# Kernel tuning notes

Hardware: AMD Instinct MI355X
Metric: run time of the kernel (lower is better)

## Reference

```python
import jax, jax.numpy as jnp
import numpy as np
from jax import lax

B, N, C, T = 8, 2000, 32, 12
K, F_CHEV, F_TIME = 3, 64, 64
LN_EPS = 1e-5


def setup_inputs() -> dict:
    key = jax.random.key(0)
    ks = jax.random.split(key, 20)
    s = 0.1
    return {
        "x": jax.random.normal(ks[0], (B, N, C, T), jnp.float32),
        "cheb_polys": jax.random.normal(ks[1], (K, N, N), jnp.float32) * 0.02,
        # temporal attention params
        "U1": jax.random.normal(ks[2], (N,), jnp.float32) * s,
        "U2": jax.random.normal(ks[3], (C, N), jnp.float32) * s,
        "U3": jax.random.normal(ks[4], (C,), jnp.float32) * s,
        "be": jax.random.normal(ks[5], (1, T, T), jnp.float32) * s,
        "Ve": jax.random.normal(ks[6], (T, T), jnp.float32) * s,
        # spatial attention params
        "W1": jax.random.normal(ks[7], (T,), jnp.float32) * s,
        "W2": jax.random.normal(ks[8], (C, T), jnp.float32) * s,
        "W3": jax.random.normal(ks[9], (C,), jnp.float32) * s,
        "bs": jax.random.normal(ks[10], (1, N, N), jnp.float32) * s,
        "Vs": jax.random.normal(ks[11], (N, N), jnp.float32) * (s / np.sqrt(N)),
        # Chebyshev conv params, stacked (K, C, F_chev)
        "Theta": jax.random.normal(ks[12], (K, C, F_CHEV), jnp.float32) * (1.0 / np.sqrt(C)),
        # time conv (1x3) and residual conv (1x1), NCHW/OIHW layout
        "tc_w": jax.random.normal(ks[13], (F_TIME, F_CHEV, 1, 3), jnp.float32) * (1.0 / np.sqrt(3 * F_CHEV)),
        "tc_b": jnp.zeros((F_TIME,), jnp.float32),
        "rc_w": jax.random.normal(ks[14], (F_TIME, C, 1, 1), jnp.float32) * (1.0 / np.sqrt(C)),
        "rc_b": jnp.zeros((F_TIME,), jnp.float32),
        # LayerNorm over nb_time_filter
        "ln_g": jnp.ones((F_TIME,), jnp.float32),
        "ln_b": jnp.zeros((F_TIME,), jnp.float32),
    }


def _conv2d(x, w, b, stride_t):
    # x: (B, Cin, N, T), w: (Cout, Cin, kh, kw)
    pad_w = (w.shape[3] - 1) // 2
    y = lax.conv_general_dilated(
        x, w, window_strides=(1, stride_t),
        padding=[(0, 0), (pad_w, pad_w)],
        dimension_numbers=("NCHW", "OIHW", "NCHW"))
    return y + b[None, :, None, None]


def reference(x, cheb_polys, U1, U2, U3, be, Ve, W1, W2, W3, bs, Vs,
              Theta, tc_w, tc_b, rc_w, rc_b, ln_g, ln_b):
    b, n, c, t = x.shape

    # ---- temporal attention: (B, T, T) ----
    lhs = jnp.einsum("bnct,n->btc", x, U1)              # x.permute(0,3,2,1) @ U1
    lhs = jnp.einsum("btc,cn->btn", lhs, U2)
    rhs = jnp.einsum("c,bnct->bnt", U3, x)
    E = jnp.einsum("ij,bjk->bik", Ve,
                   jax.nn.sigmoid(jnp.einsum("btn,bnu->btu", lhs, rhs) + be))
    temporal_At = jax.nn.softmax(E, axis=1)             # (B, T, T)

    # apply temporal attention
    x_TAt = jnp.matmul(x.reshape(b, n * c, t), temporal_At).reshape(b, n, c, t)

    # ---- spatial attention on x_TAt: (B, N, N) ----
    lhs_s = jnp.einsum("bnct,t->bnc", x_TAt, W1)
    lhs_s = jnp.einsum("bnc,ct->bnt", lhs_s, W2)
    rhs_s = jnp.einsum("c,bnct->btn", W3, x_TAt)        # (W3 @ x).transpose(-1,-2)
    S = jnp.einsum("ij,bjk->bik", Vs,
                   jax.nn.sigmoid(jnp.einsum("bnt,btm->bnm", lhs_s, rhs_s) + bs))
    spatial_At = jax.nn.softmax(S, axis=1)              # (B, N, N)

    # ---- Chebyshev graph conv with spatial attention ----
    # A[b,k,j,i] = cheb[k,j,i] * SAt[b,j,i]; out = relu(sum_k A^T x Theta_k)
    A = cheb_polys[None, :, :, :] * spatial_At[:, None, :, :]   # (B, K, N, N)
    h = jnp.einsum("bkji,bjct->bkitc", A, x)                    # (B, K, N, T, C)
    spatial_gcn = jax.nn.relu(jnp.einsum("bkitc,kcf->bift", h, Theta))  # (B, N, F, T)

    # ---- temporal conv + residual + LayerNorm ----
    time_out = _conv2d(spatial_gcn.transpose(0, 2, 1, 3), tc_w, tc_b, 1)  # (B, F_time, N, T')
    x_res = _conv2d(x.transpose(0, 2, 1, 3), rc_w, rc_b, 1)               # (B, F_time, N, T')
    z = jax.nn.relu(x_res + time_out).transpose(0, 3, 2, 1)               # (B, T', N, F_time)

    mu = jnp.mean(z, axis=-1, keepdims=True)
    var = jnp.mean((z - mu) ** 2, axis=-1, keepdims=True)
    zn = (z - mu) * lax.rsqrt(var + LN_EPS) * ln_g + ln_b

    return zn.transpose(0, 2, 3, 1)                                       # (B, N, F_time, T')
```

## Files before the change

kernel.cpp:

```cpp
#include <hip/hip_runtime.h>
#include <hip/hip_bf16.h>
#include <math.h>

#define B_ 8
#define N_ 2000
#define C_ 32
#define T_ 12
#define K_ 3
#define FC_ 64
#define FT_ 64
#define PW 2048

typedef short bf16x8 __attribute__((ext_vector_type(8)));
typedef float f32x4 __attribute__((ext_vector_type(4)));

__device__ __forceinline__ float sigmoidf(float v) { return 1.0f / (1.0f + __expf(-v)); }
__device__ __forceinline__ float bf2f(unsigned short u) {
    union { unsigned int i; float f; } v; v.i = ((unsigned int)u) << 16; return v.f;
}
__device__ __forceinline__ unsigned short f2bf(float f) {
    union { __hip_bfloat16 h; unsigned short u; } v; v.h = __float2bfloat16(f); return v.u;
}
typedef const __attribute__((address_space(1))) void* gas_t;
typedef __attribute__((address_space(3))) void* las_t;
__device__ __forceinline__ void gload16(const unsigned short* g, unsigned short* l) {
    __builtin_amdgcn_global_load_lds((gas_t)g, (las_t)l, 16, 0, 0);
}

__global__ __launch_bounds__(256) void k_tprep(const float* __restrict__ x, const float* __restrict__ U1,
                                               const float* __restrict__ U3,
                                               float* __restrict__ rhsT, float* __restrict__ plh) {
    int b = blockIdx.y, chunk = blockIdx.x;
    int tid = threadIdx.x;
    int nl = tid >> 5, c = tid & 31;
    int w = tid >> 6;
    float u3 = U3[c];
    float plA[12];
#pragma unroll
    for (int t = 0; t < 12; ++t) plA[t] = 0.f;
    for (int it = 0; it < 5; ++it) {
        int n = chunk * 40 + it * 8 + nl;
        const float* xp = x + ((size_t)(b * 2000 + n) * 32 + c) * 12;
        float4 v0 = *(const float4*)xp, v1 = *(const float4*)(xp + 4), v2 = *(const float4*)(xp + 8);
        float xv[12] = {v0.x, v0.y, v0.z, v0.w, v1.x, v1.y, v1.z, v1.w, v2.x, v2.y, v2.z, v2.w};
        float rv[12];
#pragma unroll
        for (int t = 0; t < 12; ++t) rv[t] = u3 * xv[t];
#pragma unroll
        for (int off = 16; off >= 1; off >>= 1)
#pragma unroll
            for (int t = 0; t < 12; ++t) rv[t] += __shfl_xor(rv[t], off);
        if (c == 0) {
#pragma unroll
            for (int t = 0; t < 12; ++t) rhsT[(size_t)(b * 2000 + n) * 12 + t] = rv[t];
        }
        float u1 = U1[n];
#pragma unroll
        for (int t = 0; t < 12; ++t) plA[t] += u1 * xv[t];
    }
#pragma unroll
    for (int t = 0; t < 12; ++t) plA[t] += __shfl_xor(plA[t], 32);
    __shared__ float accs[4][32][12];
    if ((tid & 63) < 32) {
#pragma unroll
        for (int t = 0; t < 12; ++t) accs[w][c][t] = plA[t];
    }
    __syncthreads();
    if (tid < 384) {
        int c2 = tid / 12, t2 = tid % 12;
        float s = accs[0][c2][t2] + accs[1][c2][t2] + accs[2][c2][t2] + accs[3][c2][t2];
        plh[((size_t)(b * 50 + chunk)) * 384 + tid] = s;
    }
}

__global__ __launch_bounds__(256) void k_tred(const float* __restrict__ plh, float* __restrict__ lhs1) {
    int b = blockIdx.x;
    for (int q = threadIdx.x; q < 384; q += 256) {
        const float* p = plh + (size_t)b * 50 * 384 + q;
        float s = 0.f;
        for (int ch = 0; ch < 50; ++ch) s += p[(size_t)ch * 384];
        int c = q / 12, t = q % 12;
        lhs1[(b * 12 + t) * 32 + c] = s;
    }
}

__global__ __launch_bounds__(256) void k_lhsT(const float* __restrict__ lhs1, const float* __restrict__ U2,
                                              float* __restrict__ lhsT) {
    int gid = blockIdx.x * 256 + threadIdx.x;
    if (gid >= B_ * T_ * N_) return;
    int n = gid % N_;
    int bt = gid / N_;
    const float* l1 = lhs1 + bt * C_;
    float a = 0.f;
#pragma unroll
    for (int c = 0; c < C_; ++c) a += l1[c] * U2[c * N_ + n];
    lhsT[gid] = a;
}

__global__ __launch_bounds__(256) void k_tatt1(const float* __restrict__ lhsT, const float* __restrict__ rhsT,
                                               float* __restrict__ pP) {
    int b = blockIdx.y, ch = blockIdx.x;
    int tid = threadIdx.x;
    int n0 = ch * 125;
    __shared__ float sL[12][128];
    __shared__ float sR[128][12];
    for (int q = tid; q < 12 * 125; q += 256) {
        int t = q / 125, nn = q % 125;
        sL[t][nn] = lhsT[(size_t)(b * 12 + t) * 2000 + n0 + nn];
    }
    for (int q = tid; q < 125 * 12; q += 256) {
        int nn = q / 12, t = q % 12;
        sR[nn][t] = rhsT[(size_t)(b * 2000 + n0 + nn) * 12 + t];
    }
    __syncthreads();
    if (tid < 144) {
        int tP = tid / 12, uP = tid % 12;
        float a = 0.f;
#pragma unroll 5
        for (int nn = 0; nn < 125; ++nn) a += sL[tP][nn] * sR[nn][uP];
        pP[(size_t)(b * 16 + ch) * 144 + tid] = a;
    }
}

__global__ __launch_bounds__(256) void k_tatt2(const float* __restrict__ pP, const float* __restrict__ be,
                                               const float* __restrict__ Ve, float* __restrict__ At) {
    int b = blockIdx.x, tid = threadIdx.x;
    __shared__ float sp[144], sE[144], mk[12], sk[12];
    int tP = tid / 12, uP = tid % 12;
    if (tid < 144) {
        float a = 0.f;
#pragma unroll
        for (int ch = 0; ch < 16; ++ch) a += pP[(size_t)(b * 16 + ch) * 144 + tid];
        sp[tid] = sigmoidf(a + be[tid]);
    }
    __syncthreads();
    if (tid < 144) {
        float e = 0.f;
#pragma unroll
        for (int j = 0; j < 12; ++j) e += Ve[tP * 12 + j] * sp[j * 12 + uP];
        sE[tid] = e;
    }
    __syncthreads();
    if (tid < 12) {
        float m = -1e30f;
#pragma unroll
        for (int i = 0; i < 12; ++i) m = fmaxf(m, sE[i * 12 + tid]);
        float s = 0.f;
#pragma unroll
        for (int i = 0; i < 12; ++i) s += __expf(sE[i * 12 + tid] - m);
        mk[tid] = m; sk[tid] = 1.0f / s;
    }
    __syncthreads();
    if (tid < 144) At[b * 144 + tid] = __expf(sE[tid] - mk[uP]) * sk[uP];
}

__global__ __launch_bounds__(256) void k_xsp(const float* __restrict__ x, const float* __restrict__ At,
                                             const float* __restrict__ W1, const float* __restrict__ W2,
                                             const float* __restrict__ W3,
                                             float* __restrict__ lhs_s, float* __restrict__ rhs_s) {
    int b = blockIdx.y, chunk = blockIdx.x;
    int tid = threadIdx.x, nl = tid >> 5, c = tid & 31;
    int n = chunk * 8 + nl;
    __shared__ float atl[144];
    __shared__ float w2l[384];
    __shared__ float w1l[12];
    if (tid < 144) atl[tid] = At[b * 144 + tid];
    if (tid >= 144 && tid < 156) w1l[tid - 144] = W1[tid - 144];
    for (int q = tid; q < 384; q += 256) w2l[q] = W2[q];
    __syncthreads();
    const float* xp = x + ((size_t)(b * 2000 + n) * 32 + c) * 12;
    float4 v0 = *(const float4*)xp, v1 = *(const float4*)(xp + 4), v2 = *(const float4*)(xp + 8);
    float xv[12] = {v0.x, v0.y, v0.z, v0.w, v1.x, v1.y, v1.z, v1.w, v2.x, v2.y, v2.z, v2.w};
    float xa[12];
#pragma unroll
    for (int t = 0; t < 12; ++t) {
        float s = 0.f;
#pragma unroll
        for (int u = 0; u < 12; ++u) s += xv[u] * atl[u * 12 + t];
        xa[t] = s;
    }
    float w3 = W3[c];
    float rv[12], lv[12];
    float l1 = 0.f;
#pragma unroll
    for (int t = 0; t < 12; ++t) l1 += xa[t] * w1l[t];
#pragma unroll
    for (int t = 0; t < 12; ++t) { rv[t] = w3 * xa[t]; lv[t] = l1 * w2l[c * 12 + t]; }
#pragma unroll
    for (int off = 16; off >= 1; off >>= 1)
#pragma unroll
        for (int t = 0; t < 12; ++t) { rv[t] += __shfl_xor(rv[t], off); lv[t] += __shfl_xor(lv[t], off); }
    if (c == 0) {
#pragma unroll
        for (int t = 0; t < 12; ++t) rhs_s[(size_t)(b * 12 + t) * 2000 + n] = rv[t];
#pragma unroll
        for (int t = 0; t < 12; ++t) lhs_s[(size_t)(b * 2000 + n) * 12 + t] = lv[t];
    }
}

__global__ __launch_bounds__(256) void k_wprep(const float* __restrict__ tc_w, const float* __restrict__ rc_w,
                                               float* __restrict__ tcwT, float* __restrict__ rcwT) {
    int gid = blockIdx.x * 256 + threadIdx.x;
    if (gid < 12288) {
        int fi = gid / 192, rem = gid % 192, f = rem / 3, d = rem % 3;
        tcwT[gid] = tc_w[(f * 64 + fi) * 3 + d];
    } else if (gid < 14336) {
        int q = gid - 12288;
        int c = q >> 6, f = q & 63;
        rcwT[q] = rc_w[f * 32 + c];
    }
}

__global__ __launch_bounds__(256) void k_vsb(const float* __restrict__ Vs, unsigned short* __restrict__ Vsb) {
    int gid = blockIdx.x * 256 + threadIdx.x;
    int row = gid >> 8, chunk = gid & 255;
    int p0 = chunk * 8;
    unsigned short o[8];
#pragma unroll
    for (int e = 0; e < 8; ++e) {
        int p = p0 + e;
        o[e] = (row < N_ && p < N_) ? f2bf(Vs[row * N_ + p]) : (unsigned short)0;
    }
    *(int4*)(Vsb + (size_t)row * PW + p0) = *(int4*)o;
}

__global__ __launch_bounds__(256) void k_chebT(const float* __restrict__ cheb, unsigned short* __restrict__ chebT) {
    int j0 = blockIdx.x * 64, i0 = blockIdx.y * 64, kk = blockIdx.z;
    __shared__ float Tl[64][65];
    int t = threadIdx.x;
    int rr = t >> 2, c0 = (t & 3) * 16;
    int j = j0 + rr;
#pragma unroll
    for (int e = 0; e < 16; ++e) {
        int i = i0 + c0 + e;
        Tl[rr][c0 + e] = (j < N_ && i < N_) ? cheb[(size_t)kk * 4000000 + (size_t)j * N_ + i] : 0.f;
    }
    __syncthreads();
    int l = t & 63, w = t >> 6;
    unsigned short o[16];
#pragma unroll
    for (int e = 0; e < 16; ++e) o[e] = f2bf(Tl[w * 16 + e][l]);
    unsigned short* dst = chebT + (size_t)kk * PW * PW + (size_t)(i0 + l) * PW + j0 + w * 16;
    *(int4*)dst = *(int4*)o;
    *(int4*)(dst + 8) = *(int4*)(o + 8);
}

__global__ __launch_bounds__(256) void k_xT(const float* __restrict__ x, unsigned short* __restrict__ xT) {
    int j0 = blockIdx.x * 64, r0 = blockIdx.y * 64, b = blockIdx.z;
    __shared__ float Tl[64][65];
    int t = threadIdx.x;
    int rr = t >> 2, c0 = (t & 3) * 16;
    int j = j0 + rr;
#pragma unroll
    for (int e = 0; e < 16; ++e) {
        int r = r0 + c0 + e;
        Tl[rr][c0 + e] = (j < N_) ? x[(size_t)(b * N_ + j) * 384 + r] : 0.f;
    }
    __syncthreads();
    int l = t & 63, w = t >> 6;
    unsigned short o[16];
#pragma unroll
    for (int e = 0; e < 16; ++e) o[e] = f2bf(Tl[w * 16 + e][l]);
    unsigned short* dst = xT + (size_t)b * 384 * PW + (size_t)(r0 + l) * PW + j0 + w * 16;
    *(int4*)dst = *(int4*)o;
    *(int4*)(dst + 8) = *(int4*)(o + 8);
}

__global__ __launch_bounds__(256) void k_sig(const float* __restrict__ lhs_s, const float* __restrict__ rhs_s,
                                             const float* __restrict__ bs, unsigned short* __restrict__ sigT) {
    int p0 = blockIdx.x * 64, i0 = blockIdx.y * 64, b = blockIdx.z;
    __shared__ float sL[64][12];
    __shared__ float sR[12][64];
    __shared__ float bsl[64][65];
    int t = threadIdx.x;
    for (int q = t; q < 768; q += 256) {
        int pp = q / 12, tt = q % 12;
        int p = p0 + pp;
        sL[pp][tt] = (p < N_) ? lhs_s[(b * N_ + p) * 12 + tt] : 0.f;
    }
    for (int q = t; q < 768; q += 256) {
        int tt = q >> 6, ii = q & 63;
        int i = i0 + ii;
        sR[tt][ii] = (i < N_) ? rhs_s[b * (T_ * N_) + tt * N_ + i] : 0.f;
    }
    {
        int pp = t >> 2, c0 = (t & 3) * 16;
        int p = p0 + pp;
        if (p < N_ && i0 + c0 + 15 < N_) {
            const float* src = bs + (size_t)p * N_ + i0 + c0;
#pragma unroll
            for (int e = 0; e < 16; e += 4) *(float4*)&bsl[pp][c0 + e] = *(const float4*)(src + e);
        } else {
#pragma unroll
            for (int e = 0; e < 16; ++e) {
                int i = i0 + c0 + e;
                bsl[pp][c0 + e] = (p < N_ && i < N_) ? bs[(size_t)p * N_ + i] : 0.f;
            }
        }
    }
    __syncthreads();
    int ii = t & 63, w = t >> 6;
    int i = i0 + ii;
    unsigned short o[16];
#pragma unroll
    for (int e = 0; e < 16; ++e) {
        int pl = w * 16 + e;
        int p = p0 + pl;
        float v = 0.f;
        if (p < N_ && i < N_) {
            float d = bsl[pl][ii];
#pragma unroll
            for (int tt = 0; tt < 12; ++tt) d += sL[pl][tt] * sR[tt][ii];
            v = sigmoidf(d);
        }
        o[e] = f2bf(v);
    }
    unsigned short* dst = sigT + (size_t)b * PW * PW + (size_t)i * PW + p0 + w * 16;
    *(int4*)dst = *(int4*)o;
    *(int4*)(dst + 8) = *(int4*)(o + 8);
}

__global__ __launch_bounds__(512) void k_gemm_S_mfma(const unsigned short* __restrict__ Vsb,
                                                     const unsigned short* __restrict__ sigT,
                                                     unsigned short* __restrict__ ST) {
    int lid = blockIdx.x + (blockIdx.y << 3) + (blockIdx.z << 6);
    int swz = (lid & 7) * 64 + (lid >> 3);
    int j0 = (swz & 7) * 256;
    int i0 = ((swz >> 3) & 7) * 256;
    int b = swz >> 6;
    const unsigned short* Ap = sigT + (size_t)b * PW * PW;
    __shared__ unsigned short As[2][16384];
    __shared__ unsigned short Bs[2][16384];
    int t = threadIdx.x, lane = t & 63, w = t >> 6;
    int wr = w >> 2, wc = w & 3;
    int l15 = lane & 15, kseg = lane >> 4;
    f32x4 acc[8][4];
#pragma unroll
    for (int m = 0; m < 8; ++m)
#pragma unroll
        for (int n = 0; n < 4; ++n)
#pragma unroll
            for (int q = 0; q < 4; ++q) acc[m][n][q] = 0.f;
    int srow = t >> 3;
    int schunk = ((t & 7) ^ (srow & 7)) * 8;
    const unsigned short* gA = Ap + (size_t)(i0 + srow) * PW + schunk;
    const unsigned short* gB = Vsb + (size_t)(j0 + srow) * PW + schunk;
    int ldw = w * 512;
#define SA_(buf_, kt_, h_) do { \
    gload16(gA + (size_t)((h_) * 128) * PW + (kt_) * 64, &As[buf_][(h_) * 8192 + ldw]); \
    gload16(gA + (size_t)((h_) * 128 + 64) * PW + (kt_) * 64, &As[buf_][(h_) * 8192 + 4096 + ldw]); \
} while (0)
#define SB_(buf_, kt_, h_) do { \
    gload16(gB + (size_t)((h_) * 128) * PW + (kt_) * 64, &Bs[buf_][(h_) * 8192 + ldw]); \
    gload16(gB + (size_t)((h_) * 128 + 64) * PW + (kt_) * 64, &Bs[buf_][(h_) * 8192 + 4096 + ldw]); \
} while (0)
#define RDA(dst, mh_, buf_) do { \
    _Pragma("unroll") for (int m = 0; m < 4; ++m) { \
        int R = wr * 128 + (mh_) * 64 + m * 16 + l15; \
        _Pragma("unroll") for (int kh = 0; kh < 2; ++kh) \
            dst[m][kh] = *(const bf16x8*)&As[buf_][R * 64 + (((kh * 4 + kseg) ^ (R & 7)) << 3)]; \
    } } while (0)
#define RDB(dst, nh_, buf_) do { \
    _Pragma("unroll") for (int n = 0; n < 2; ++n) { \
        int R = wc * 64 + (nh_) * 32 + n * 16 + l15; \
        _Pragma("unroll") for (int kh = 0; kh < 2; ++kh) \
            dst[n][kh] = *(const bf16x8*)&Bs[buf_][R * 64 + (((kh * 4 + kseg) ^ (R & 7)) << 3)]; \
    } } while (0)
#define LGKM0 do { asm volatile("s_waitcnt lgkmcnt(0)" ::: "memory"); __builtin_amdgcn_sched_barrier(0); } while (0)
#define MMA(av, bv, mh_, nh_) do { \
    __builtin_amdgcn_s_setprio(1); \
    _Pragma("unroll") for (int m = 0; m < 4; ++m) \
    _Pragma("unroll") for (int n = 0; n < 2; ++n) \
    _Pragma("unroll") for (int kh = 0; kh < 2; ++kh) \
        acc[m + (mh_) * 4][n + (nh_) * 2] = __builtin_amdgcn_mfma_f32_16x16x32_bf16( \
            av[m][kh], bv[n][kh], acc[m + (mh_) * 4][n + (nh_) * 2], 0, 0, 0); \
    __builtin_amdgcn_s_setprio(0); } while (0)
    SA_(0, 0, 0); SA_(0, 0, 1); SB_(0, 0, 0); SB_(0, 0, 1);
    for (int kt = 0; kt < 32; ++kt) {
        int buf = kt & 1, nbuf = buf ^ 1;
        bf16x8 aR[4][2], bR[2][2];
        asm volatile("s_waitcnt vmcnt(0)" ::: "memory");
        __builtin_amdgcn_s_barrier();
        __builtin_amdgcn_sched_barrier(0);
        if (kt + 1 < 32) { SA_(nbuf, kt + 1, 0); SA_(nbuf, kt + 1, 1); }
        RDA(aR, 0, buf); RDB(bR, 0, buf);
        LGKM0;
        MMA(aR, bR, 0, 0);
        __builtin_amdgcn_s_barrier();
        if (kt + 1 < 32) { SB_(nbuf, kt + 1, 0); SB_(nbuf, kt + 1, 1); }
        RDB(bR, 1, buf);
        LGKM0;
        MMA(aR, bR, 0, 1);
        __builtin_amdgcn_s_barrier();
        RDA(aR, 1, buf); RDB(bR, 0, buf);
        LGKM0;
        MMA(aR, bR, 1, 0);
        __builtin_amdgcn_s_barrier();
        RDB(bR, 1, buf);
        LGKM0;
        MMA(aR, bR, 1, 1);
    }
#undef SA_
#undef SB_
#undef RDA
#undef RDB
#undef LGKM0
#undef MMA
    unsigned short* Sp = ST + (size_t)b * PW * PW;
#pragma unroll
    for (int mi = 0; mi < 8; ++mi) {
        int row0 = i0 + wr * 128 + (mi >> 2) * 64 + (mi & 3) * 16 + (kseg << 2);
#pragma unroll
        for (int ni = 0; ni < 4; ++ni) {
            int col = j0 + wc * 64 + (ni >> 1) * 32 + (ni & 1) * 16 + l15;
#pragma unroll
            for (int q = 0; q < 4; ++q)
                Sp[(size_t)(row0 + q) * PW + col] = f2bf(acc[mi][ni][q]);
        }
    }
}

__global__ __launch_bounds__(256) void k_smrow(const unsigned short* __restrict__ ST,
                                               float* __restrict__ gm, float* __restrict__ gs) {
    int wid = threadIdx.x >> 6, lane = threadIdx.x & 63;
    int b = blockIdx.y;
    int i = blockIdx.x * 4 + wid;
    const unsigned short* rp = ST + (size_t)b * PW * PW + (size_t)i * PW;
    float vals[32];
    float m = -1e30f;
#pragma unroll
    for (int k = 0; k < 4; ++k) {
        int j0 = lane * 8 + k * 512;
        if (j0 < N_) {
            union { int4 v; unsigned short s[8]; } u;
            u.v = *(const int4*)(rp + j0);
#pragma unroll
            for (int e = 0; e < 8; ++e) {
                vals[k * 8 + e] = bf2f(u.s[e]);
                m = fmaxf(m, vals[k * 8 + e]);
            }
        } else {
#pragma unroll
            for (int e = 0; e < 8; ++e) vals[k * 8 + e] = -1e30f;
        }
    }
#pragma unroll
    for (int off = 32; off >= 1; off >>= 1) m = fmaxf(m, __shfl_xor(m, off));
    float s = 0.f;
#pragma unroll
    for (int k = 0; k < 32; ++k) s += __expf(vals[k] - m);
#pragma unroll
    for (int off = 32; off >= 1; off >>= 1) s += __shfl_xor(s, off);
    if (lane == 0) {
        gm[b * 2048 + i] = m;
        gs[b * 2048 + i] = 1.0f / s;
    }
}

__global__ __launch_bounds__(512) void k_gemm_cheb_mfma(const unsigned short* __restrict__ chebT,
                                                        const unsigned short* __restrict__ ST,
                                                        const float* __restrict__ gm, const float* __restrict__ gs,
                                                        const unsigned short* __restrict__ xT,
                                                        unsigned short* __restrict__ h2) {
    int bk = blockIdx.y;
    int b = bk / 3, kk = bk % 3;
    int i0 = blockIdx.x * 128;
    const unsigned short* Ac = chebT + (size_t)kk * PW * PW;
    const unsigned short* Sa = ST + (size_t)b * PW * PW;
    const unsigned short* Bx = xT + (size_t)b * 384 * PW;
    __shared__ unsigned short As[2][4096];
    __shared__ unsigned short Bs[2][12288];
    int t = threadIdx.x, lane = t & 63, w = t >> 6;
    int wr = w >> 2, wc = w & 3;
    f32x4 acc[4][6];
#pragma unroll
    for (int a = 0; a < 4; ++a)
#pragma unroll
        for (int c = 0; c < 6; ++c)
#pragma unroll
            for (int q = 0; q < 4; ++q) acc[a][c][q] = 0.f;
    int arow = t >> 2, aq = t & 3;
    const unsigned short* gc = Ac + (size_t)(i0 + arow) * PW + aq * 8;
    const unsigned short* gsat = Sa + (size_t)(i0 + arow) * PW + aq * 8;
    float gmv = gm[b * 2048 + i0 + arow];
    float gsv = gs[b * 2048 + i0 + arow];
    int aoff = arow * 32 + (aq ^ (arow & 3)) * 8;
    int bseg = (t & 3) ^ ((t >> 2) & 3);
    const unsigned short* gB = Bx + (size_t)(t >> 2) * PW + bseg * 8;
    int ldso = w * 512;
#define STAGE_B(buf, p) do { \
    gload16(gB + (p), &Bs[buf][ldso]); \
    gload16(gB + 128 * PW + (p), &Bs[buf][4096 + ldso]); \
    gload16(gB + 256 * PW + (p), &Bs[buf][8192 + ldso]); \
} while (0)
    union U8 { int4 v; unsigned short s[8]; };
    U8 ca, sa;
    ca.v = *(const int4*)gc;
    sa.v = *(const int4*)gsat;
    STAGE_B(0, 0);
    {
        U8 o;
#pragma unroll
        for (int e = 0; e < 8; ++e) o.s[e] = f2bf(bf2f(ca.s[e]) * __expf(bf2f(sa.s[e]) - gmv) * gsv);
        *(int4*)&As[0][aoff] = o.v;
    }
    ca.v = *(const int4*)(gc + 32);
    sa.v = *(const int4*)(gsat + 32);
    __syncthreads();
    int cur = 0;
    int rswz = ((lane >> 4) ^ (lane & 3)) * 8;
    for (int p = 0; p < PW; p += 32) {
        if (p + 32 < PW) {
            STAGE_B(cur ^ 1, p + 32);
            U8 o;
#pragma unroll
            for (int e = 0; e < 8; ++e) o.s[e] = f2bf(bf2f(ca.s[e]) * __expf(bf2f(sa.s[e]) - gmv) * gsv);
            *(int4*)&As[cur ^ 1][aoff] = o.v;
            int pn = (p + 64 < PW) ? p + 64 : 0;
            ca.v = *(const int4*)(gc + pn);
            sa.v = *(const int4*)(gsat + pn);
        }
        bf16x8 af[4], bfr[6];
#pragma unroll
        for (int fm = 0; fm < 4; ++fm)
            af[fm] = *(const bf16x8*)&As[cur][(wr * 64 + fm * 16 + (lane & 15)) * 32 + rswz];
#pragma unroll
        for (int fn = 0; fn < 6; ++fn)
            bfr[fn] = *(const bf16x8*)&Bs[cur][(wc * 96 + fn * 16 + (lane & 15)) * 32 + rswz];
#pragma unroll
        for (int fm = 0; fm < 4; ++fm)
#pragma unroll
            for (int fn = 0; fn < 6; ++fn)
                acc[fm][fn] = __builtin_amdgcn_mfma_f32_16x16x32_bf16(af[fm], bfr[fn], acc[fm][fn], 0, 0, 0);
        __syncthreads();
        cur ^= 1;
    }
#undef STAGE_B
    unsigned short* hp = h2 + (size_t)bk * 768000;
#pragma unroll
    for (int fm = 0; fm < 4; ++fm) {
        int row0 = i0 + wr * 64 + fm * 16 + ((lane >> 4) << 2);
#pragma unroll
        for (int fn = 0; fn < 6; ++fn) {
            int col = wc * 96 + fn * 16 + (lane & 15);
#pragma unroll
            for (int q = 0; q < 4; ++q) {
                int row = row0 + q;
                if (row < N_) hp[(size_t)row * 384 + col] = f2bf(acc[fm][fn][q]);
            }
        }
    }
}

__global__ __launch_bounds__(512) void k_final3(const float* __restrict__ x, const unsigned short* __restrict__ h2,
                                                const float* __restrict__ ThetaG,
                                                const float* __restrict__ tcwT, const float* __restrict__ tc_b,
                                                const float* __restrict__ rcwT, const float* __restrict__ rc_b,
                                                const float* __restrict__ ln_g, const float* __restrict__ ln_b,
                                                float* __restrict__ out) {
    __shared__ __align__(16) char smem[110848];
    unsigned int* gl = (unsigned int*)smem;
    unsigned short* th = (unsigned short*)(smem + 98560);
    float* red_s = (float*)(smem + 98560);
    float* red_q = red_s + 64 * 13;

    int tid = threadIdx.x;
    int n_l = tid & 63, fg = tid >> 6;
    int b = blockIdx.y;
    int node = blockIdx.x * 64 + n_l;
    bool ok = node < N_;
    int nd = ok ? node : N_ - 1;

    for (int q = tid; q < 6144; q += 512) th[q] = f2bf(ThetaG[q]);
    __syncthreads();

    float acc[8][12];
#pragma unroll
    for (int ff = 0; ff < 8; ++ff)
#pragma unroll
        for (int t = 0; t < 12; ++t) acc[ff][t] = 0.f;
    const unsigned short* hb = h2 + (size_t)b * 3 * 768000 + (size_t)nd * 384;
#pragma unroll
    for (int kk = 0; kk < 3; ++kk) {
        const unsigned short* hp = hb + (size_t)kk * 768000;
#pragma unroll 2
        for (int c = 0; c < 32; ++c) {
            const unsigned short* hq = hp + c * 12;
            uint2 u0 = *(const uint2*)(hq);
            uint2 u1 = *(const uint2*)(hq + 4);
            uint2 u2 = *(const uint2*)(hq + 8);
            float h[12];
            h[0] = bf2f((unsigned short)u0.x);  h[1] = bf2f((unsigned short)(u0.x >> 16));
            h[2] = bf2f((unsigned short)u0.y);  h[3] = bf2f((unsigned short)(u0.y >> 16));
            h[4] = bf2f((unsigned short)u1.x);  h[5] = bf2f((unsigned short)(u1.x >> 16));
            h[6] = bf2f((unsigned short)u1.y);  h[7] = bf2f((unsigned short)(u1.y >> 16));
            h[8] = bf2f((unsigned short)u2.x);  h[9] = bf2f((unsigned short)(u2.x >> 16));
            h[10] = bf2f((unsigned short)u2.y); h[11] = bf2f((unsigned short)(u2.y >> 16));
            const unsigned short* wv = th + (kk * 32 + c) * 64 + fg * 8;
            uint2 w01 = *(const uint2*)wv;
            uint2 w23 = *(const uint2*)(wv + 4);
            float wf[8];
            wf[0] = bf2f((unsigned short)w01.x); wf[1] = bf2f((unsigned short)(w01.x >> 16));
            wf[2] = bf2f((unsigned short)w01.y); wf[3] = bf2f((unsigned short)(w01.y >> 16));
            wf[4] = bf2f((unsigned short)w23.x); wf[5] = bf2f((unsigned short)(w23.x >> 16));
            wf[6] = bf2f((unsigned short)w23.y); wf[7] = bf2f((unsigned short)(w23.y >> 16));
#pragma unroll
            for (int ff = 0; ff < 8; ++ff)
#pragma unroll
                for (int t = 0; t < 12; ++t) acc[ff][t] = fmaf(h[t], wf[ff], acc[ff][t]);
        }
    }
    unsigned int* gr = gl + n_l * 385 + fg * 48;
#pragma unroll
    for (int ff = 0; ff < 8; ++ff)
#pragma unroll
        for (int tp = 0; tp < 6; ++tp) {
            float a0 = fmaxf(acc[ff][2 * tp], 0.f), a1 = fmaxf(acc[ff][2 * tp + 1], 0.f);
            gr[ff * 6 + tp] = (unsigned int)f2bf(a0) | ((unsigned int)f2bf(a1) << 16);
        }
    __syncthreads();

    float z[8][12];
#pragma unroll
    for (int ff = 0; ff < 8; ++ff) {
        float bias = tc_b[fg * 8 + ff] + rc_b[fg * 8 + ff];
#pragma unroll
        for (int t = 0; t < 12; ++t) z[ff][t] = bias;
    }
    const float* xp = x + (size_t)(b * 2000 + nd) * 384;
#pragma unroll 2
    for (int c = 0; c < 32; ++c) {
        float4 x0 = *(const float4*)(xp + c * 12);
        float4 x1 = *(const float4*)(xp + c * 12 + 4);
        float4 x2 = *(const float4*)(xp + c * 12 + 8);
        float xv[12] = {x0.x, x0.y, x0.z, x0.w, x1.x, x1.y, x1.z, x1.w, x2.x, x2.y, x2.z, x2.w};
        float4 r0 = *(const float4*)(rcwT + c * 64 + fg * 8);
        float4 r1 = *(const float4*)(rcwT + c * 64 + fg * 8 + 4);
        float rw[8] = {r0.x, r0.y, r0.z, r0.w, r1.x, r1.y, r1.z, r1.w};
#pragma unroll
        for (int ff = 0; ff < 8; ++ff)
#pragma unroll
            for (int t = 0; t < 12; ++t) z[ff][t] = fmaf(xv[t], rw[ff], z[ff][t]);
    }
    const unsigned int* grow = gl + n_l * 385;
    for (int fi = 0; fi < 64; ++fi) {
        float g[12];
#pragma unroll
        for (int j = 0; j < 6; ++j) {
            unsigned int u = grow[fi * 6 + j];
            g[2 * j] = bf2f((unsigned short)u);
            g[2 * j + 1] = bf2f((unsigned short)(u >> 16));
        }
        const float* wp = tcwT + (fi * 64 + fg * 8) * 3;
        float4 w0 = *(const float4*)(wp);
        float4 w1 = *(const float4*)(wp + 4);
        float4 w2 = *(const float4*)(wp + 8);
        float4 w3 = *(const float4*)(wp + 12);
        float4 w4 = *(const float4*)(wp + 16);
        float4 w5 = *(const float4*)(wp + 20);
        float wb[24] = {w0.x, w0.y, w0.z, w0.w, w1.x, w1.y, w1.z, w1.w,
                        w2.x, w2.y, w2.z, w2.w, w3.x, w3.y, w3.z, w3.w,
                        w4.x, w4.y, w4.z, w4.w, w5.x, w5.y, w5.z, w5.w};
#pragma unroll
        for (int ff = 0; ff < 8; ++ff) {
            float a0 = wb[ff * 3], a1 = wb[ff * 3 + 1], a2 = wb[ff * 3 + 2];
            z[ff][0] = fmaf(g[0], a1, fmaf(g[1], a2, z[ff][0]));
#pragma unroll
            for (int t = 1; t < 11; ++t)
                z[ff][t] = fmaf(g[t - 1], a0, fmaf(g[t], a1, fmaf(g[t + 1], a2, z[ff][t])));
            z[ff][11] = fmaf(g[10], a0, fmaf(g[11], a1, z[ff][11]));
        }
    }
#pragma unroll
    for (int ff = 0; ff < 8; ++ff)
#pragma unroll
        for (int t = 0; t < 12; ++t) z[ff][t] = fmaxf(z[ff][t], 0.f);

    float s[12], q[12];
#pragma unroll
    for (int t = 0; t < 12; ++t) { s[t] = 0.f; q[t] = 0.f; }
#pragma unroll
    for (int ff = 0; ff < 8; ++ff)
#pragma unroll
        for (int t = 0; t < 12; ++t) { s[t] += z[ff][t]; q[t] += z[ff][t] * z[ff][t]; }
    __syncthreads();
    for (int g = 0; g < 8; ++g) {
        if (fg == g) {
            if (g == 0) {
#pragma unroll
                for (int t = 0; t < 12; ++t) { red_s[n_l * 13 + t] = s[t]; red_q[n_l * 13 + t] = q[t]; }
            } else {
#pragma unroll
                for (int t = 0; t < 12; ++t) { red_s[n_l * 13 + t] += s[t]; red_q[n_l * 13 + t] += q[t]; }
            }
        }
        __syncthreads();
    }
    float mu[12], rs[12];
#pragma unroll
    for (int t = 0; t < 12; ++t) {
        float m = red_s[n_l * 13 + t] * (1.0f / 64.0f);
        float v = red_q[n_l * 13 + t] * (1.0f / 64.0f) - m * m;
        mu[t] = m;
        rs[t] = rsqrtf(v + 1e-5f);
    }
    if (ok) {
        float* op = out + ((size_t)(b * 2000 + node) * 64 + fg * 8) * 12;
#pragma unroll
        for (int ff = 0; ff < 8; ++ff) {
            float lg = ln_g[fg * 8 + ff], lb = ln_b[fg * 8 + ff];
            float o[12];
#pragma unroll
            for (int t = 0; t < 12; ++t) o[t] = (z[ff][t] - mu[t]) * rs[t] * lg + lb;
#pragma unroll
            for (int tq = 0; tq < 3; ++tq)
                *(float4*)(op + ff * 12 + tq * 4) = make_float4(o[tq * 4], o[tq * 4 + 1], o[tq * 4 + 2], o[tq * 4 + 3]);
        }
    }
}

extern "C" void kernel_launch(void* const* d_in, const int* in_sizes, int n_in,
                              void* d_out, int out_size, void* d_ws, size_t ws_size,
                              hipStream_t stream) {
    const float* x     = (const float*)d_in[0];
    const float* cheb  = (const float*)d_in[1];
    const float* U1    = (const float*)d_in[2];
    const float* U2    = (const float*)d_in[3];
    const float* U3    = (const float*)d_in[4];
    const float* be    = (const float*)d_in[5];
    const float* Ve    = (const float*)d_in[6];
    const float* W1    = (const float*)d_in[7];
    const float* W2    = (const float*)d_in[8];
    const float* W3    = (const float*)d_in[9];
    const float* bs    = (const float*)d_in[10];
    const float* Vs    = (const float*)d_in[11];
    const float* Theta = (const float*)d_in[12];
    const float* tc_w  = (const float*)d_in[13];
    const float* tc_b  = (const float*)d_in[14];
    const float* rc_w  = (const float*)d_in[15];
    const float* rc_b  = (const float*)d_in[16];
    const float* ln_g  = (const float*)d_in[17];
    const float* ln_b  = (const float*)d_in[18];
    float* out = (float*)d_out;

    float* ws    = (float*)d_ws;
    float* At    = ws;
    float* lhs1  = ws + 1152;
    float* lhsT  = ws + 4224;
    float* rhsT  = ws + 196224;
    float* lhs_s = ws + 388224;
    float* rhs_s = ws + 580224;
    float* gm    = ws + 772224;
    float* gs    = ws + 788608;
    float* tcwT  = ws + 804992;
    float* rcwT  = ws + 817280;
    float* plh   = ws + 819328;
    float* pP    = ws + 972928;
    unsigned short* Vsb   = (unsigned short*)(ws + 991360);
    unsigned short* chebT = (unsigned short*)(ws + 3088512);
    unsigned short* xT    = (unsigned short*)(ws + 9379968);
    unsigned short* sigT  = (unsigned short*)(ws + 12525696);
    unsigned short* h2    = sigT;
    unsigned short* STb   = (unsigned short*)(ws + 29302912);

    k_wprep<<<56, 256, 0, stream>>>(tc_w, rc_w, tcwT, rcwT);
    k_vsb<<<2048, 256, 0, stream>>>(Vs, Vsb);
    k_chebT<<<dim3(32, 32, 3), 256, 0, stream>>>(cheb, chebT);
    k_xT<<<dim3(32, 6, 8), 256, 0, stream>>>(x, xT);
    k_tprep<<<dim3(50, 8), 256, 0, stream>>>(x, U1, U3, rhsT, plh);
    k_tred<<<8, 256, 0, stream>>>(plh, lhs1);
    k_lhsT<<<750, 256, 0, stream>>>(lhs1, U2, lhsT);
    k_tatt1<<<dim3(16, 8), 256, 0, stream>>>(lhsT, rhsT, pP);
    k_tatt2<<<8, 256, 0, stream>>>(pP, be, Ve, At);
    k_xsp<<<dim3(250, 8), 256, 0, stream>>>(x, At, W1, W2, W3, lhs_s, rhs_s);
    k_sig<<<dim3(32, 32, 8), 256, 0, stream>>>(lhs_s, rhs_s, bs, sigT);
    k_gemm_S_mfma<<<dim3(8, 8, 8), 512, 0, stream>>>(Vsb, sigT, STb);
    k_smrow<<<dim3(512, 8), 256, 0, stream>>>(STb, gm, gs);
    k_gemm_cheb_mfma<<<dim3(16, 24), 512, 0, stream>>>(chebT, STb, gm, gs, xT, h2);
    k_final3<<<dim3(32, 8), 512, 0, stream>>>(x, h2, Theta, tcwT, tc_b, rcwT, rc_b, ln_g, ln_b, out);
}
```

Baseline: 637.4 us.

## Split S GEMM LDS tiles by K-half and deepen prefetch pipeline

```diff
diff --git a/kernel.cpp b/kernel.cpp
--- a/kernel.cpp
+++ b/kernel.cpp
@@ -320,6 +320,7 @@
     *(int4*)(dst + 8) = *(int4*)(o + 8);
 }
 
+#define FR_(R) (((R) ^ ((R) >> 2)) & 3)
 __global__ __launch_bounds__(512) void k_gemm_S_mfma(const unsigned short* __restrict__ Vsb,
                                                      const unsigned short* __restrict__ sigT,
                                                      unsigned short* __restrict__ ST) {
@@ -329,8 +330,8 @@
     int i0 = ((swz >> 3) & 7) * 256;
     int b = swz >> 6;
     const unsigned short* Ap = sigT + (size_t)b * PW * PW;
-    __shared__ unsigned short As[2][16384];
-    __shared__ unsigned short Bs[2][16384];
+    __shared__ unsigned short As[2][2][8192];
+    __shared__ unsigned short Bs[2][2][8192];
     int t = threadIdx.x, lane = t & 63, w = t >> 6;
     int wr = w >> 2, wc = w & 3;
     int l15 = lane & 15, kseg = lane >> 4;
@@ -341,64 +342,64 @@
         for (int n = 0; n < 4; ++n)
 #pragma unroll
             for (int q = 0; q < 4; ++q) acc[m][n][q] = 0.f;
-    int srow = t >> 3;
-    int schunk = ((t & 7) ^ (srow & 7)) * 8;
-    const unsigned short* gA = Ap + (size_t)(i0 + srow) * PW + schunk;
-    const unsigned short* gB = Vsb + (size_t)(j0 + srow) * PW + schunk;
+    int srow = t >> 2;
+    int gchunk = ((t & 3) ^ FR_(srow)) * 8;
+    const unsigned short* gA = Ap + (size_t)(i0 + srow) * PW + gchunk;
+    const unsigned short* gB = Vsb + (size_t)(j0 + srow) * PW + gchunk;
     int ldw = w * 512;
-#define SA_(buf_, kt_, h_) do { \
-    gload16(gA + (size_t)((h_) * 128) * PW + (kt_) * 64, &As[buf_][(h_) * 8192 + ldw]); \
-    gload16(gA + (size_t)((h_) * 128 + 64) * PW + (kt_) * 64, &As[buf_][(h_) * 8192 + 4096 + ldw]); \
+#define SA_(buf_, kt_, kh_) do { \
+    gload16(gA + (size_t)(kt_) * 64 + (kh_) * 32, &As[buf_][kh_][ldw]); \
+    gload16(gA + (size_t)128 * PW + (size_t)(kt_) * 64 + (kh_) * 32, &As[buf_][kh_][4096 + ldw]); \
 } while (0)
-#define SB_(buf_, kt_, h_) do { \
-    gload16(gB + (size_t)((h_) * 128) * PW + (kt_) * 64, &Bs[buf_][(h_) * 8192 + ldw]); \
-    gload16(gB + (size_t)((h_) * 128 + 64) * PW + (kt_) * 64, &Bs[buf_][(h_) * 8192 + 4096 + ldw]); \
+#define SB_(buf_, kt_, kh_) do { \
+    gload16(gB + (size_t)(kt_) * 64 + (kh_) * 32, &Bs[buf_][kh_][ldw]); \
+    gload16(gB + (size_t)128 * PW + (size_t)(kt_) * 64 + (kh_) * 32, &Bs[buf_][kh_][4096 + ldw]); \
 } while (0)
-#define RDA(dst, mh_, buf_) do { \
-    _Pragma("unroll") for (int m = 0; m < 4; ++m) { \
-        int R = wr * 128 + (mh_) * 64 + m * 16 + l15; \
-        _Pragma("unroll") for (int kh = 0; kh < 2; ++kh) \
-            dst[m][kh] = *(const bf16x8*)&As[buf_][R * 64 + (((kh * 4 + kseg) ^ (R & 7)) << 3)]; \
-    } } while (0)
-#define RDB(dst, nh_, buf_) do { \
-    _Pragma("unroll") for (int n = 0; n < 2; ++n) { \
-        int R = wc * 64 + (nh_) * 32 + n * 16 + l15; \
-        _Pragma("unroll") for (int kh = 0; kh < 2; ++kh) \
-            dst[n][kh] = *(const bf16x8*)&Bs[buf_][R * 64 + (((kh * 4 + kseg) ^ (R & 7)) << 3)]; \
-    } } while (0)
+#define RDA(kh_, buf_) { _Pragma("unroll") for (int m = 0; m < 8; ++m) { \
+    int R = wr * 128 + m * 16 + l15; \
+    aR[m] = *(const bf16x8*)&As[buf_][kh_][R * 32 + ((kseg ^ FR_(R)) << 3)]; } }
+#define RDB(kh_, nh_, buf_) { _Pragma("unroll") for (int n = 0; n < 2; ++n) { \
+    int R = wc * 64 + (nh_) * 32 + n * 16 + l15; \
+    bR[n] = *(const bf16x8*)&Bs[buf_][kh_][R * 32 + ((kseg ^ FR_(R)) << 3)]; } }
 #define LGKM0 do { asm volatile("s_waitcnt lgkmcnt(0)" ::: "memory"); __builtin_amdgcn_sched_barrier(0); } while (0)
-#define MMA(av, bv, mh_, nh_) do { \
-    __builtin_amdgcn_s_setprio(1); \
-    _Pragma("unroll") for (int m = 0; m < 4; ++m) \
+#define MMA(nh_) do { __builtin_amdgcn_s_setprio(1); \
+    _Pragma("unroll") for (int m = 0; m < 8; ++m) \
     _Pragma("unroll") for (int n = 0; n < 2; ++n) \
-    _Pragma("unroll") for (int kh = 0; kh < 2; ++kh) \
-        acc[m + (mh_) * 4][n + (nh_) * 2] = __builtin_amdgcn_mfma_f32_16x16x32_bf16( \
-            av[m][kh], bv[n][kh], acc[m + (mh_) * 4][n + (nh_) * 2], 0, 0, 0); \
+        acc[m][(nh_) * 2 + n] = __builtin_amdgcn_mfma_f32_16x16x32_bf16(aR[m], bR[n], acc[m][(nh_) * 2 + n], 0, 0, 0); \
     __builtin_amdgcn_s_setprio(0); } while (0)
-    SA_(0, 0, 0); SA_(0, 0, 1); SB_(0, 0, 0); SB_(0, 0, 1);
+    SA_(0, 0, 0); SB_(0, 0, 0); SA_(0, 0, 1); SB_(0, 0, 1);
+    SA_(1, 1, 0); SB_(1, 1, 0);
+    asm volatile("s_waitcnt vmcnt(4)" ::: "memory");
+    __builtin_amdgcn_s_barrier();
     for (int kt = 0; kt < 32; ++kt) {
-        int buf = kt & 1, nbuf = buf ^ 1;
-        bf16x8 aR[4][2], bR[2][2];
-        asm volatile("s_waitcnt vmcnt(0)" ::: "memory");
+        int cur = kt & 1, nb = cur ^ 1;
+        bf16x8 aR[8], bR[2];
+        RDA(0, cur); RDB(0, 0, cur);
+        if (kt + 1 < 32) SA_(nb, kt + 1, 1);
         __builtin_amdgcn_s_barrier();
-        __builtin_amdgcn_sched_barrier(0);
-        if (kt + 1 < 32) { SA_(nbuf, kt + 1, 0); SA_(nbuf, kt + 1, 1); }
-        RDA(aR, 0, buf); RDB(bR, 0, buf);
         LGKM0;
-        MMA(aR, bR, 0, 0);
+        MMA(0);
         __builtin_amdgcn_s_barrier();
-        if (kt + 1 < 32) { SB_(nbuf, kt + 1, 0); SB_(nbuf, kt + 1, 1); }
-        RDB(bR, 1, buf);
+        RDB(0, 1, cur);
+        if (kt + 1 < 32) SB_(nb, kt + 1, 1);
+        __builtin_amdgcn_s_barrier();
         LGKM0;
-        MMA(aR, bR, 0, 1);
+        MMA(1);
         __builtin_amdgcn_s_barrier();
-        RDA(aR, 1, buf); RDB(bR, 0, buf);
+        RDA(1, cur); RDB(1, 0, cur);
+        if (kt + 2 < 32) SA_(cur, kt + 2, 0);
+        __builtin_amdgcn_s_barrier();
         LGKM0;
-        MMA(aR, bR, 1, 0);
+        MMA(0);
         __builtin_amdgcn_s_barrier();
-        RDB(bR, 1, buf);
+        RDB(1, 1, cur);
+        if (kt + 2 < 32) SB_(cur, kt + 2, 0);
+        __builtin_amdgcn_s_barrier();
         LGKM0;
-        MMA(aR, bR, 1, 1);
+        MMA(1);
+        if (kt < 30) asm volatile("s_waitcnt vmcnt(4)" ::: "memory");
+        else         asm volatile("s_waitcnt vmcnt(0)" ::: "memory");
+        __builtin_amdgcn_s_barrier();
     }
 #undef SA_
 #undef SB_
@@ -408,14 +409,14 @@
 #undef MMA
     unsigned short* Sp = ST + (size_t)b * PW * PW;
 #pragma unroll
-    for (int mi = 0; mi < 8; ++mi) {
-        int row0 = i0 + wr * 128 + (mi >> 2) * 64 + (mi & 3) * 16 + (kseg << 2);
-#pragma unroll
-        for (int ni = 0; ni < 4; ++ni) {
-            int col = j0 + wc * 64 + (ni >> 1) * 32 + (ni & 1) * 16 + l15;
+    for (int m = 0; m < 8; ++m) {
+        int row0 = i0 + wr * 128 + m * 16 + (kseg << 2);
+#pragma unroll
+        for (int n = 0; n < 4; ++n) {
+            int col = j0 + wc * 64 + (n >> 1) * 32 + (n & 1) * 16 + l15;
 #pragma unroll
             for (int q = 0; q < 4; ++q)
-                Sp[(size_t)(row0 + q) * PW + col] = f2bf(acc[mi][ni][q]);
+                Sp[(size_t)(row0 + q) * PW + col] = f2bf(acc[m][n][q]);
         }
     }
 }
```

Measured after the change: 603.6 us. -5.3%, faster.
